# Optimization experiments

Hardware: AMD Instinct MI355X
Metric: run time of the kernel (lower is better)

The kernel has to match this reference:

```python
import jax, jax.numpy as jnp
import numpy as np

B, P, G, E = 2, 16, 128, 96
C110, C011, C001 = 4, 2, 1
N, CO = 128, 2

def _pw(x, W, b):
    """1x1 conv of any spatial rank == pointwise channel mixing."""
    y = jnp.einsum('oc,bc...->bo...', W, x)
    return y + b.reshape((1, -1) + (1,) * (y.ndim - 2))

def _hidden(s110, s011, s001, Ws, bs):
    # s110:[B,C,P,G,1]  s011:[B,C,1,G,E]  s001:[B,C,1,1,E]
    # sub-stream order: [110 full, 110 pool-P, 110 pool-G, 011 full, 011 pool-G, 011 pool-E, 001]
    t110 = s110[..., 0]         # [B,C,P,G]
    t011 = s011[:, :, 0]        # [B,C,G,E]
    t001 = s001[:, :, 0, 0]     # [B,C,E]
    s = (_pw(t110, Ws[0], bs[0])[..., None]
         + _pw(t110.max(axis=2), Ws[1], bs[1])[:, :, None, :, None]
         + _pw(t110.max(axis=3), Ws[2], bs[2])[:, :, :, None, None]
         + _pw(t011, Ws[3], bs[3])[:, :, None, :, :]
         + _pw(t011.max(axis=2), Ws[4], bs[4])[:, :, None, None, :]
         + _pw(t011.max(axis=3), Ws[5], bs[5])[:, :, None, :, None]
         + _pw(t001, Ws[6], bs[6])[:, :, None, None, :])
    s = jax.nn.leaky_relu(s)    # [B,N,P,G,E]
    return (jnp.max(s, axis=4, keepdims=True),
            jnp.max(s, axis=2, keepdims=True),
            jnp.max(s, axis=(2, 3), keepdims=True))

def _forward(x110, x011, x001, W0_110, b0_110, W0_011, b0_011, W0_001, b0_001, W1, b1, Wact, bact, Wcrit, bcrit):
    Ws0 = [W0_110[0], W0_110[1], W0_110[2], W0_011[0], W0_011[1], W0_011[2], W0_001]
    bs0 = [b0_110[0], b0_110[1], b0_110[2], b0_011[0], b0_011[1], b0_011[2], b0_001]
    s110, s011, s001 = _hidden(x110, x011, x001, Ws0, bs0)
    s110, s011, s001 = _hidden(s110, s011, s001, list(W1), list(b1))
    t110 = s110[..., 0]  # [B,N,P,G]
    # actor head: eliminate G,E via mean pooling (dim_elimination_max_pooling=False)
    a110 = _pw(t110.mean(axis=3), Wact[0], bact[0])              # [B,CO,P]
    a011 = _pw(s011.mean(axis=(3, 4)), Wact[1], bact[1])         # [B,CO,1]
    a001 = _pw(s001[:, :, :, 0].mean(axis=3), Wact[2], bact[2])  # [B,CO,1]
    actions = jax.nn.leaky_relu(a110 + a011 + a001)              # [B,CO,P]
    # critic head: eliminate G via mean pooling
    c110 = _pw(t110.mean(axis=3), Wcrit[0], bcrit[0])            # [B,CO,P]
    c011 = _pw(s011[:, :, 0].mean(axis=2), Wcrit[1], bcrit[1])   # [B,CO,E]
    c001 = _pw(s001[:, :, 0, 0], Wcrit[2], bcrit[2])             # [B,CO,E]
    v = jax.nn.leaky_relu(c110[:, :, :, None] + (c011 + c001)[:, :, None, :])  # [B,CO,P,E]
    v110 = v.max(axis=3).sum(axis=2)  # stream (1,1,0): max over E, sum over P
    v011 = v.max(axis=2).sum(axis=2)  # streams (0,1,1) and (0,0,1) coincide numerically
    values = (2.0 + v110 + 2.0 * v011).reshape(-1)  # python sum(l, 2) starts at 2
    return actions, values

def setup_inputs() -> dict:
    key = jax.random.key(0)
    ks = jax.random.split(key, 12)
    f32 = jnp.float32
    def w(k, shape, fan):
        return jax.random.normal(k, shape, f32) / np.float32(np.sqrt(fan))
    return {
        'x110': jax.random.normal(ks[0], (B, C110, P, G, 1), f32),
        'x011': jax.random.normal(ks[1], (B, C011, 1, G, E), f32),
        'x001': jax.random.normal(ks[2], (B, C001, 1, 1, E), f32),
        'W0_110': w(ks[3], (3, N, C110), C110), 'b0_110': jnp.zeros((3, N), f32),
        'W0_011': w(ks[4], (3, N, C011), C011), 'b0_011': jnp.zeros((3, N), f32),
        'W0_001': w(ks[5], (N, C001), C001),    'b0_001': jnp.zeros((N,), f32),
        'W1':     w(ks[6], (7, N, N), N),       'b1':     jnp.zeros((7, N), f32),
        'Wact':   w(ks[7], (3, CO, N), N),      'bact':   jnp.zeros((3, CO), f32),
        'Wcrit':  w(ks[8], (3, CO, N), N),      'bcrit':  jnp.zeros((3, CO), f32),
    }

def reference(x110, x011, x001, W0_110, b0_110, W0_011, b0_011, W0_001, b0_001, W1, b1, Wact, bact, Wcrit, bcrit):
    return _forward(x110, x011, x001, W0_110, b0_110, W0_011, b0_011, W0_001, b0_001, W1, b1, Wact, bact, Wcrit, bcrit)
```

## Files before the change

### kernel.cpp

```cpp
#include <hip/hip_runtime.h>
#include <math.h>

#define DEVI __device__ __forceinline__

constexpr int B = 2, P = 16, G = 128, E = 96, N = 128, CO = 2;

DEVI float lrelu(float x) { return x > 0.f ? x : 0.01f * x; }
DEVI float4 lrelu4(float4 v) {
  return make_float4(lrelu(v.x), lrelu(v.y), lrelu(v.z), lrelu(v.w));
}

constexpr int OFF_U0     = 0;
constexpr int OFF_V0     = OFF_U0 + 524288;
constexpr int OFF_S110   = OFF_V0 + 3145728;
constexpr int OFF_MAXPU0 = OFF_S110 + 524288;
constexpr int OFF_MP110  = OFF_MAXPU0 + 32768;
constexpr int OFF_MG110  = OFF_MP110 + 32768;
constexpr int OFF_S001A  = OFF_MG110 + 4096;
constexpr int OFF_C1P    = OFF_S001A + 24576;
constexpr int OFF_BF1G   = OFF_C1P + 4096;
constexpr int OFF_EG1E   = OFF_BF1G + 32768;
constexpr int OFF_U1     = OFF_EG1E + 24576;
constexpr int OFF_V1     = OFF_U1 + 524288;
constexpr int OFF_M110   = OFF_V1 + 3145728;
constexpr int OFF_M011E  = OFF_M110 + 4096;
constexpr int OFF_S001B  = OFF_M011E + 24576;

__global__ void k_in_reduce(const float* __restrict__ x110,
                            const float* __restrict__ x011,
                            float* __restrict__ rmp110, float* __restrict__ rmg110,
                            float* __restrict__ rme011, float* __restrict__ rmg011) {
  int t = blockIdx.x * 256 + threadIdx.x;
  if (t < 1024) {
    int g = t & 127, c = (t >> 7) & 3, b = t >> 9;
    const float* base = x110 + ((b * 4 + c) * P) * G + g;
    float m = -INFINITY;
    for (int p = 0; p < P; p++) m = fmaxf(m, base[p * G]);
    rmp110[t] = m;
  } else if (t < 1152) {
    int i = t - 1024;
    int p = i & 15, c = (i >> 4) & 3, b = i >> 6;
    const float* base = x110 + ((b * 4 + c) * P + p) * G;
    float m = -INFINITY;
    for (int g = 0; g < G; g++) m = fmaxf(m, base[g]);
    rmg110[i] = m;
  } else if (t < 1664) {
    int i = t - 1152;
    int g = i & 127, c = (i >> 7) & 1, b = i >> 8;
    const float* base = x011 + ((b * 2 + c) * G + g) * E;
    float m = -INFINITY;
    for (int e = 0; e < E; e++) m = fmaxf(m, base[e]);
    rme011[i] = m;
  } else if (t < 2048) {
    int i = t - 1664;
    int e = i % 96; int r = i / 96; int c = r & 1, b = r >> 1;
    const float* base = x011 + ((b * 2 + c) * G) * E + e;
    float m = -INFINITY;
    for (int g = 0; g < G; g++) m = fmaxf(m, base[g * E]);
    rmg011[i] = m;
  }
}

__global__ void k_UV0(const float* __restrict__ x110, const float* __restrict__ x011,
                      const float* __restrict__ x001,
                      const float* __restrict__ W0_110, const float* __restrict__ b0_110,
                      const float* __restrict__ W0_011, const float* __restrict__ b0_011,
                      const float* __restrict__ W0_001, const float* __restrict__ b0_001,
                      const float* __restrict__ rmp110, const float* __restrict__ rmg110,
                      const float* __restrict__ rme011, const float* __restrict__ rmg011,
                      float* __restrict__ U, float* __restrict__ V) {
  int blk = blockIdx.x;
  if (blk < 2048) {
    int t = blk * 256 + threadIdx.x;
    int g = t & 127, p = (t >> 7) & 15, n = (t >> 11) & 127, b = t >> 18;
    float acc = b0_110[n] + b0_110[N + n] + b0_110[2 * N + n] + b0_011[2 * N + n];
#pragma unroll
    for (int c = 0; c < 4; c++) {
      acc += W0_110[n * 4 + c]           * x110[((b * 4 + c) * P + p) * G + g];
      acc += W0_110[(N + n) * 4 + c]     * rmp110[(b * 4 + c) * G + g];
      acc += W0_110[(2 * N + n) * 4 + c] * rmg110[(b * 4 + c) * P + p];
    }
#pragma unroll
    for (int c = 0; c < 2; c++)
      acc += W0_011[(2 * N + n) * 2 + c] * rme011[(b * 2 + c) * G + g];
    U[t] = acc;
  } else {
    int t = (blk - 2048) * 256 + threadIdx.x;
    int e = t % 96; int r = t / 96;
    int g = r & 127, n = (r >> 7) & 127, b = r >> 14;
    float acc = b0_011[n] + b0_011[N + n] + b0_001[n];
#pragma unroll
    for (int c = 0; c < 2; c++) {
      acc += W0_011[n * 2 + c]       * x011[((b * 2 + c) * G + g) * E + e];
      acc += W0_011[(N + n) * 2 + c] * rmg011[(b * 2 + c) * E + e];
    }
    acc += W0_001[n] * x001[b * E + e];
    V[t] = acc;
  }
}

__global__ void __launch_bounds__(256) k_post0(
    const float* __restrict__ U, const float* __restrict__ V,
    float* __restrict__ s110, float* __restrict__ maxpU0,
    float* __restrict__ mp110, float* __restrict__ mg110,
    float* __restrict__ s001a) {
  __shared__ float uU[P * G];
  __shared__ float part[256];
  __shared__ float smaxeV[G], smaxpU[G];
  const int bn = blockIdx.x;
  const int tid = threadIdx.x;
  const float4* usrc = (const float4*)(U + (size_t)bn * P * G);
  float4* udst = (float4*)uU;
  udst[tid] = usrc[tid];
  udst[tid + 256] = usrc[tid + 256];
  {
    int g = tid & 127, h = tid >> 7;
    const float* vrow = V + ((size_t)bn * G + g) * E + h * 48;
    float m = -INFINITY;
#pragma unroll
    for (int j = 0; j < 12; j++) {
      float4 v = *(const float4*)(vrow + j * 4);
      m = fmaxf(m, fmaxf(fmaxf(v.x, v.y), fmaxf(v.z, v.w)));
    }
    part[tid] = m;
  }
  __syncthreads();
  if (tid < G) {
    smaxeV[tid] = fmaxf(part[tid], part[tid + 128]);
    float mp = -INFINITY;
    for (int p = 0; p < P; p++) mp = fmaxf(mp, uU[p * G + tid]);
    smaxpU[tid] = mp;
    maxpU0[bn * G + tid] = mp;
  }
  __syncthreads();
  {
    float4* sdst = (float4*)(s110 + (size_t)bn * P * G);
#pragma unroll
    for (int k = 0; k < 2; k++) {
      int i = tid + k * 256;
      int g4 = i & 31;
      float4 u = ((float4*)uU)[i];
      float4 mv = *(float4*)&smaxeV[g4 * 4];
      sdst[i] = make_float4(lrelu(u.x + mv.x), lrelu(u.y + mv.y),
                            lrelu(u.z + mv.z), lrelu(u.w + mv.w));
    }
  }
  if (tid < G)
    mp110[bn * G + tid] = lrelu(smaxpU[tid] + smaxeV[tid]);
  if (tid < P) {
    float mm = -INFINITY;
    for (int g = 0; g < G; g++) mm = fmaxf(mm, uU[tid * G + g] + smaxeV[g]);
    mg110[bn * P + tid] = lrelu(mm);
  }
  if (tid < E) {
    float mm = -INFINITY;
    const float* vcol = V + (size_t)bn * G * E + tid;
    for (int g = 0; g < G; g++) mm = fmaxf(mm, smaxpU[g] + vcol[g * E]);
    s001a[bn * E + tid] = lrelu(mm);
  }
}

__global__ void k_sg(const float* __restrict__ W1, const float* __restrict__ mp110,
                     const float* __restrict__ mg110, const float* __restrict__ s001a,
                     float* __restrict__ C1p, float* __restrict__ BF1g,
                     float* __restrict__ EG1e) {
  int t = blockIdx.x * 256 + threadIdx.x;
  if (t < 4096) {
    int p = t & 15, n = (t >> 4) & 127, b = t >> 11;
    float acc = 0.f;
    for (int c = 0; c < N; c++)
      acc += W1[(2 * N + n) * N + c] * mg110[(b * N + c) * P + p];
    C1p[t] = acc;
  } else if (t < 36864) {
    int i = t - 4096;
    int g = i & 127, n = (i >> 7) & 127, b = i >> 14;
    float acc = 0.f;
    for (int c = 0; c < N; c++)
      acc += (W1[(1 * N + n) * N + c] + W1[(5 * N + n) * N + c])
             * mp110[(b * N + c) * G + g];
    BF1g[i] = acc;
  } else {
    int i = t - 36864;
    int e = i % 96; int r = i / 96; int n = r & 127, b = r >> 7;
    float acc = 0.f;
    for (int c = 0; c < N; c++)
      acc += (W1[(4 * N + n) * N + c] + W1[(6 * N + n) * N + c])
             * s001a[(b * N + c) * E + e];
    EG1e[i] = acc;
  }
}

__global__ void __launch_bounds__(256) k_V1U1(
    const float* __restrict__ V0, const float* __restrict__ maxpU0,
    const float* __restrict__ s110, const float* __restrict__ W1,
    const float* __restrict__ b1, const float* __restrict__ C1p,
    const float* __restrict__ BF1g, const float* __restrict__ EG1e,
    float* __restrict__ U1, float* __restrict__ V1) {
  __shared__ float sS[N * E];
  const int blk = blockIdx.x;
  const int tid = threadIdx.x;
  if (blk < 256) {
    const int g = blk & 127, b = blk >> 7;
    for (int i4 = tid; i4 < N * E / 4; i4 += 256) {
      int c = i4 / 24, e4 = i4 - c * 24;
      float4 v = *(const float4*)(V0 + ((size_t)(b * N + c) * G + g) * E + e4 * 4);
      float mp = maxpU0[(b * N + c) * G + g];
      *(float4*)&sS[c * E + e4 * 4] =
          make_float4(lrelu(v.x + mp), lrelu(v.y + mp),
                      lrelu(v.z + mp), lrelu(v.w + mp));
    }
    __syncthreads();
    const int e12 = tid & 7, n4 = tid >> 3;
    const int n0 = n4 * 4, e0 = e12 * 12;
    float4 acc[4][3];
#pragma unroll
    for (int ni = 0; ni < 4; ni++) {
      int n = n0 + ni;
      float bb = b1[3 * N + n] + b1[4 * N + n] + b1[6 * N + n];
      const float* eg = EG1e + (b * N + n) * E + e0;
#pragma unroll
      for (int k = 0; k < 3; k++)
        acc[ni][k] = make_float4(bb + eg[k * 4], bb + eg[k * 4 + 1],
                                 bb + eg[k * 4 + 2], bb + eg[k * 4 + 3]);
    }
    for (int c = 0; c < N; c += 4) {
      float4 wv[4];
#pragma unroll
      for (int ni = 0; ni < 4; ni++)
        wv[ni] = *(const float4*)&W1[(size_t)(3 * N + n0 + ni) * N + c];
#pragma unroll
      for (int cc = 0; cc < 4; cc++) {
        float4 s0 = *(float4*)&sS[(c + cc) * E + e0];
        float4 s1 = *(float4*)&sS[(c + cc) * E + e0 + 4];
        float4 s2 = *(float4*)&sS[(c + cc) * E + e0 + 8];
#pragma unroll
        for (int ni = 0; ni < 4; ni++) {
          float wc = cc == 0 ? wv[ni].x : cc == 1 ? wv[ni].y : cc == 2 ? wv[ni].z : wv[ni].w;
          acc[ni][0].x += wc * s0.x; acc[ni][0].y += wc * s0.y;
          acc[ni][0].z += wc * s0.z; acc[ni][0].w += wc * s0.w;
          acc[ni][1].x += wc * s1.x; acc[ni][1].y += wc * s1.y;
          acc[ni][1].z += wc * s1.z; acc[ni][1].w += wc * s1.w;
          acc[ni][2].x += wc * s2.x; acc[ni][2].y += wc * s2.y;
          acc[ni][2].z += wc * s2.z; acc[ni][2].w += wc * s2.w;
        }
      }
    }
#pragma unroll
    for (int ni = 0; ni < 4; ni++) {
      float* dst = V1 + ((size_t)(b * N + n0 + ni) * G + g) * E + e0;
#pragma unroll
      for (int k = 0; k < 3; k++) *(float4*)(dst + k * 4) = acc[ni][k];
    }
  } else {
    int t = (blk - 256) * 256 + tid;
    int g4 = t & 31, p = (t >> 5) & 15, n4 = (t >> 9) & 31, b = t >> 14;
    int n0 = n4 * 4;
    float4 a[4];
#pragma unroll
    for (int ni = 0; ni < 4; ni++) {
      int n = n0 + ni;
      float bb = b1[n] + b1[N + n] + b1[2 * N + n] + b1[5 * N + n]
               + C1p[(b * N + n) * P + p];
      float4 bf = *(const float4*)&BF1g[(b * N + n) * G + g4 * 4];
      a[ni] = make_float4(bb + bf.x, bb + bf.y, bb + bf.z, bb + bf.w);
    }
#pragma unroll 4
    for (int c = 0; c < N; c++) {
      float4 v = *(const float4*)&s110[((size_t)(b * N + c) * P + p) * G + g4 * 4];
#pragma unroll
      for (int ni = 0; ni < 4; ni++) {
        float wc = W1[(size_t)(n0 + ni) * N + c];
        a[ni].x += wc * v.x; a[ni].y += wc * v.y;
        a[ni].z += wc * v.z; a[ni].w += wc * v.w;
      }
    }
#pragma unroll
    for (int ni = 0; ni < 4; ni++)
      *(float4*)&U1[((size_t)(b * N + n0 + ni) * P + p) * G + g4 * 4] = a[ni];
  }
}

__global__ void __launch_bounds__(256) k_post1(
    const float* __restrict__ U1, const float* __restrict__ V1,
    float* __restrict__ m110, float* __restrict__ m011e,
    float* __restrict__ s001b) {
  __shared__ float uU[P * G];
  __shared__ float part[256];
  __shared__ float smaxeV[G], smaxpU[G];
  const int bn = blockIdx.x;
  const int tid = threadIdx.x;
  const float4* usrc = (const float4*)(U1 + (size_t)bn * P * G);
  float4* udst = (float4*)uU;
  udst[tid] = usrc[tid];
  udst[tid + 256] = usrc[tid + 256];
  {
    int g = tid & 127, h = tid >> 7;
    const float* vrow = V1 + ((size_t)bn * G + g) * E + h * 48;
    float m = -INFINITY;
#pragma unroll
    for (int j = 0; j < 12; j++) {
      float4 v = *(const float4*)(vrow + j * 4);
      m = fmaxf(m, fmaxf(fmaxf(v.x, v.y), fmaxf(v.z, v.w)));
    }
    part[tid] = m;
  }
  __syncthreads();
  if (tid < G) {
    smaxeV[tid] = fmaxf(part[tid], part[tid + 128]);
    float mp = -INFINITY;
    for (int p = 0; p < P; p++) mp = fmaxf(mp, uU[p * G + tid]);
    smaxpU[tid] = mp;
  }
  __syncthreads();
  if (tid < P) {
    float s = 0.f;
    for (int g = 0; g < G; g++) s += lrelu(uU[tid * G + g] + smaxeV[g]);
    m110[bn * P + tid] = s * (1.f / G);
  }
  if (tid < E) {
    float s = 0.f, mm = -INFINITY;
    const float* vcol = V1 + (size_t)bn * G * E + tid;
    for (int g = 0; g < G; g++) {
      float pre = smaxpU[g] + vcol[g * E];
      s += lrelu(pre);
      mm = fmaxf(mm, pre);
    }
    m011e[bn * E + tid] = s * (1.f / G);
    s001b[bn * E + tid] = lrelu(mm);
  }
}

__global__ void __launch_bounds__(128) k_final(const float* __restrict__ m110,
                                               const float* __restrict__ m011e,
                                               const float* __restrict__ s001,
                                               const float* __restrict__ Wact,
                                               const float* __restrict__ bact,
                                               const float* __restrict__ Wcrit,
                                               const float* __restrict__ bcrit,
                                               float* __restrict__ out) {
  __shared__ float sm011[N], sm001[N], scp[P], sce[E], srow[P], scol[E];
  const int bo = blockIdx.x;
  const int o = bo & 1, b = bo >> 1;
  const int t = threadIdx.x;
  {
    float s1 = 0.f, s2 = 0.f;
    const float* p1 = m011e + (b * N + t) * E;
    const float* p2 = s001 + (b * N + t) * E;
    for (int e = 0; e < E; e++) { s1 += p1[e]; s2 += p2[e]; }
    sm011[t] = s1 * (1.f / E);
    sm001[t] = s2 * (1.f / E);
  }
  __syncthreads();
  if (t < P) {
    const float* wa0 = Wact + o * N;
    const float* wa1 = Wact + (1 * CO + o) * N;
    const float* wa2 = Wact + (2 * CO + o) * N;
    const float* wc0 = Wcrit + o * N;
    float a = 0.f, c = 0.f, aa = 0.f;
    for (int n = 0; n < N; n++) {
      float m = m110[(b * N + n) * P + t];
      a += wa0[n] * m;
      c += wc0[n] * m;
      aa += wa1[n] * sm011[n] + wa2[n] * sm001[n];
    }
    float act = a + aa + bact[o] + bact[CO + o] + bact[2 * CO + o];
    out[(b * CO + o) * P + t] = lrelu(act);
    scp[t] = c + bcrit[o];
  } else if (t < P + E) {
    int e = t - P;
    const float* wc1 = Wcrit + (1 * CO + o) * N;
    const float* wc2 = Wcrit + (2 * CO + o) * N;
    float c = 0.f;
    for (int n = 0; n < N; n++)
      c += wc1[n] * m011e[(b * N + n) * E + e] + wc2[n] * s001[(b * N + n) * E + e];
    sce[e] = c + bcrit[CO + o] + bcrit[2 * CO + o];
  }
  __syncthreads();
  if (t < P) {
    float m = -INFINITY;
    for (int e = 0; e < E; e++) m = fmaxf(m, lrelu(scp[t] + sce[e]));
    srow[t] = m;
  } else if (t < P + E) {
    int e = t - P;
    float m = -INFINITY;
    for (int p = 0; p < P; p++) m = fmaxf(m, lrelu(scp[p] + sce[e]));
    scol[e] = m;
  }
  __syncthreads();
  if (t == 0) {
    float v110 = 0.f, v011 = 0.f;
    for (int p = 0; p < P; p++) v110 += srow[p];
    for (int e = 0; e < E; e++) v011 += scol[e];
    out[B * CO * P + b * CO + o] = 2.f + v110 + 2.f * v011;
  }
}

extern "C" void kernel_launch(void* const* d_in, const int* in_sizes, int n_in,
                              void* d_out, int out_size, void* d_ws, size_t ws_size,
                              hipStream_t stream) {
  const float* x110   = (const float*)d_in[0];
  const float* x011   = (const float*)d_in[1];
  const float* x001   = (const float*)d_in[2];
  const float* W0_110 = (const float*)d_in[3];
  const float* b0_110 = (const float*)d_in[4];
  const float* W0_011 = (const float*)d_in[5];
  const float* b0_011 = (const float*)d_in[6];
  const float* W0_001 = (const float*)d_in[7];
  const float* b0_001 = (const float*)d_in[8];
  const float* W1     = (const float*)d_in[9];
  const float* b1     = (const float*)d_in[10];
  const float* Wact   = (const float*)d_in[11];
  const float* bact   = (const float*)d_in[12];
  const float* Wcrit  = (const float*)d_in[13];
  const float* bcrit  = (const float*)d_in[14];
  float* out = (float*)d_out;
  float* w = (float*)d_ws;

  float* U0     = w + OFF_U0;
  float* V0     = w + OFF_V0;
  float* s110   = w + OFF_S110;
  float* maxpU0 = w + OFF_MAXPU0;
  float* mp110  = w + OFF_MP110;
  float* mg110  = w + OFF_MG110;
  float* s001a  = w + OFF_S001A;
  float* C1p    = w + OFF_C1P;
  float* BF1g   = w + OFF_BF1G;
  float* EG1e   = w + OFF_EG1E;
  float* U1     = w + OFF_U1;
  float* V1     = w + OFF_V1;
  float* m110   = w + OFF_M110;
  float* m011e  = w + OFF_M011E;
  float* s001b  = w + OFF_S001B;

  float* rmp110 = w + OFF_S001B + 24576;
  float* rmg110 = rmp110 + 1024;
  float* rme011 = rmg110 + 128;
  float* rmg011 = rme011 + 512;

  k_in_reduce<<<8, 256, 0, stream>>>(x110, x011, rmp110, rmg110, rme011, rmg011);
  k_UV0<<<14336, 256, 0, stream>>>(x110, x011, x001, W0_110, b0_110, W0_011,
                                   b0_011, W0_001, b0_001,
                                   rmp110, rmg110, rme011, rmg011, U0, V0);
  k_post0<<<256, 256, 0, stream>>>(U0, V0, s110, maxpU0, mp110, mg110, s001a);
  k_sg<<<240, 256, 0, stream>>>(W1, mp110, mg110, s001a, C1p, BF1g, EG1e);
  k_V1U1<<<384, 256, 0, stream>>>(V0, maxpU0, s110, W1, b1, C1p, BF1g, EG1e,
                                  U1, V1);
  k_post1<<<256, 256, 0, stream>>>(U1, V1, m110, m011e, s001b);
  k_final<<<4, 128, 0, stream>>>(m110, m011e, s001b, Wact, bact, Wcrit, bcrit, out);
}
```

Before: 125.7 us.

## Fuse layer-0 into per-(b,n) blocks and recompute layer-0 activations in layer-1

Merges the input reductions, the layer-0 pointwise U0/V0 computation and its post-processing into one kernel, so each (b,n) block builds U0/V0 in shared memory instead of writing them to global memory. The layer-1 kernel now regenerates the needed s110 and s011 slices per (b,g) from the raw inputs and the stored max vectors rather than reading the large V0 and s110 buffers. This removes roughly 15 MB of global writes and reads and two launches. In exchange the layer-0 arithmetic is recomputed, and the shared-memory footprint grows, which may limit occupancy. The U1 store is also changed to a strided scalar pattern.

Result: faster. 104.7 us (-16.7%).

```diff
diff --git a/kernel.cpp b/kernel.cpp
--- a/kernel.cpp
+++ b/kernel.cpp
@@ -6,157 +6,162 @@
 constexpr int B = 2, P = 16, G = 128, E = 96, N = 128, CO = 2;
 
 DEVI float lrelu(float x) { return x > 0.f ? x : 0.01f * x; }
-DEVI float4 lrelu4(float4 v) {
-  return make_float4(lrelu(v.x), lrelu(v.y), lrelu(v.z), lrelu(v.w));
-}
-
-constexpr int OFF_U0     = 0;
-constexpr int OFF_V0     = OFF_U0 + 524288;
-constexpr int OFF_S110   = OFF_V0 + 3145728;
-constexpr int OFF_MAXPU0 = OFF_S110 + 524288;
-constexpr int OFF_MP110  = OFF_MAXPU0 + 32768;
+
+constexpr int OFF_U1     = 0;
+constexpr int OFF_V1     = OFF_U1 + 524288;
+constexpr int OFF_MAXPU0 = OFF_V1 + 3145728;
+constexpr int OFF_MAXEV0 = OFF_MAXPU0 + 32768;
+constexpr int OFF_MP110  = OFF_MAXEV0 + 32768;
 constexpr int OFF_MG110  = OFF_MP110 + 32768;
 constexpr int OFF_S001A  = OFF_MG110 + 4096;
-constexpr int OFF_C1P    = OFF_S001A + 24576;
+constexpr int OFF_RMP    = OFF_S001A + 24576;
+constexpr int OFF_RMG    = OFF_RMP + 1024;
+constexpr int OFF_RME    = OFF_RMG + 128;
+constexpr int OFF_RMG011 = OFF_RME + 512;
+constexpr int OFF_C1P    = OFF_RMG011 + 384;
 constexpr int OFF_BF1G   = OFF_C1P + 4096;
 constexpr int OFF_EG1E   = OFF_BF1G + 32768;
-constexpr int OFF_U1     = OFF_EG1E + 24576;
-constexpr int OFF_V1     = OFF_U1 + 524288;
-constexpr int OFF_M110   = OFF_V1 + 3145728;
+constexpr int OFF_M110   = OFF_EG1E + 24576;
 constexpr int OFF_M011E  = OFF_M110 + 4096;
 constexpr int OFF_S001B  = OFF_M011E + 24576;
 
-__global__ void k_in_reduce(const float* __restrict__ x110,
-                            const float* __restrict__ x011,
-                            float* __restrict__ rmp110, float* __restrict__ rmg110,
-                            float* __restrict__ rme011, float* __restrict__ rmg011) {
-  int t = blockIdx.x * 256 + threadIdx.x;
-  if (t < 1024) {
-    int g = t & 127, c = (t >> 7) & 3, b = t >> 9;
-    const float* base = x110 + ((b * 4 + c) * P) * G + g;
-    float m = -INFINITY;
-    for (int p = 0; p < P; p++) m = fmaxf(m, base[p * G]);
-    rmp110[t] = m;
-  } else if (t < 1152) {
-    int i = t - 1024;
-    int p = i & 15, c = (i >> 4) & 3, b = i >> 6;
-    const float* base = x110 + ((b * 4 + c) * P + p) * G;
-    float m = -INFINITY;
-    for (int g = 0; g < G; g++) m = fmaxf(m, base[g]);
-    rmg110[i] = m;
-  } else if (t < 1664) {
-    int i = t - 1152;
-    int g = i & 127, c = (i >> 7) & 1, b = i >> 8;
-    const float* base = x011 + ((b * 2 + c) * G + g) * E;
-    float m = -INFINITY;
-    for (int e = 0; e < E; e++) m = fmaxf(m, base[e]);
-    rme011[i] = m;
-  } else if (t < 2048) {
-    int i = t - 1664;
-    int e = i % 96; int r = i / 96; int c = r & 1, b = r >> 1;
-    const float* base = x011 + ((b * 2 + c) * G) * E + e;
-    float m = -INFINITY;
-    for (int g = 0; g < G; g++) m = fmaxf(m, base[g * E]);
-    rmg011[i] = m;
-  }
-}
-
-__global__ void k_UV0(const float* __restrict__ x110, const float* __restrict__ x011,
-                      const float* __restrict__ x001,
-                      const float* __restrict__ W0_110, const float* __restrict__ b0_110,
-                      const float* __restrict__ W0_011, const float* __restrict__ b0_011,
-                      const float* __restrict__ W0_001, const float* __restrict__ b0_001,
-                      const float* __restrict__ rmp110, const float* __restrict__ rmg110,
-                      const float* __restrict__ rme011, const float* __restrict__ rmg011,
-                      float* __restrict__ U, float* __restrict__ V) {
-  int blk = blockIdx.x;
-  if (blk < 2048) {
-    int t = blk * 256 + threadIdx.x;
-    int g = t & 127, p = (t >> 7) & 15, n = (t >> 11) & 127, b = t >> 18;
-    float acc = b0_110[n] + b0_110[N + n] + b0_110[2 * N + n] + b0_011[2 * N + n];
-#pragma unroll
-    for (int c = 0; c < 4; c++) {
-      acc += W0_110[n * 4 + c]           * x110[((b * 4 + c) * P + p) * G + g];
-      acc += W0_110[(N + n) * 4 + c]     * rmp110[(b * 4 + c) * G + g];
-      acc += W0_110[(2 * N + n) * 4 + c] * rmg110[(b * 4 + c) * P + p];
-    }
-#pragma unroll
-    for (int c = 0; c < 2; c++)
-      acc += W0_011[(2 * N + n) * 2 + c] * rme011[(b * 2 + c) * G + g];
-    U[t] = acc;
-  } else {
-    int t = (blk - 2048) * 256 + threadIdx.x;
-    int e = t % 96; int r = t / 96;
-    int g = r & 127, n = (r >> 7) & 127, b = r >> 14;
-    float acc = b0_011[n] + b0_011[N + n] + b0_001[n];
-#pragma unroll
-    for (int c = 0; c < 2; c++) {
-      acc += W0_011[n * 2 + c]       * x011[((b * 2 + c) * G + g) * E + e];
-      acc += W0_011[(N + n) * 2 + c] * rmg011[(b * 2 + c) * E + e];
-    }
-    acc += W0_001[n] * x001[b * E + e];
-    V[t] = acc;
-  }
-}
-
-__global__ void __launch_bounds__(256) k_post0(
-    const float* __restrict__ U, const float* __restrict__ V,
-    float* __restrict__ s110, float* __restrict__ maxpU0,
+__global__ void __launch_bounds__(256) k_layer0(
+    const float* __restrict__ x110, const float* __restrict__ x011,
+    const float* __restrict__ x001,
+    const float* __restrict__ W0_110, const float* __restrict__ b0_110,
+    const float* __restrict__ W0_011, const float* __restrict__ b0_011,
+    const float* __restrict__ W0_001, const float* __restrict__ b0_001,
+    float* __restrict__ maxpU0g, float* __restrict__ maxeV0g,
     float* __restrict__ mp110, float* __restrict__ mg110,
-    float* __restrict__ s001a) {
-  __shared__ float uU[P * G];
-  __shared__ float part[256];
-  __shared__ float smaxeV[G], smaxpU[G];
-  const int bn = blockIdx.x;
-  const int tid = threadIdx.x;
-  const float4* usrc = (const float4*)(U + (size_t)bn * P * G);
-  float4* udst = (float4*)uU;
-  udst[tid] = usrc[tid];
-  udst[tid + 256] = usrc[tid + 256];
+    float* __restrict__ s001a,
+    float* __restrict__ rmpG, float* __restrict__ rmgG,
+    float* __restrict__ rmeG, float* __restrict__ rmg011G) {
+  __shared__ float xs[4 * 16 * 128];
+  __shared__ float v0[128 * 97];
+  __shared__ float u0[16 * 128];
+  __shared__ float rmp[4 * 128], rmgS[4 * 16], rme[2 * 128], rmg011L[2 * 96];
+  __shared__ float mpu[128], mev[128], part[256];
+  const int bn = blockIdx.x, b = bn >> 7, n = bn & 127, tid = threadIdx.x;
+
+  {
+    const float4* xsrc = (const float4*)(x110 + (size_t)b * 8192);
+    float4* xdst = (float4*)xs;
+#pragma unroll
+    for (int k = 0; k < 8; k++) xdst[tid + k * 256] = xsrc[tid + k * 256];
+  }
+  __syncthreads();
+  for (int i = tid; i < 512; i += 256) {
+    int c = i >> 7, g = i & 127;
+    float m = -INFINITY;
+    for (int p = 0; p < P; p++) m = fmaxf(m, xs[(c * 16 + p) * 128 + g]);
+    rmp[i] = m;
+  }
+  if (tid < 64) {
+    int c = tid >> 4, p = tid & 15;
+    float m = -INFINITY;
+    for (int g = 0; g < G; g++) m = fmaxf(m, xs[(c * 16 + p) * 128 + g]);
+    rmgS[tid] = m;
+  }
+  {
+    int c = tid >> 7, g = tid & 127;
+    const float4* r = (const float4*)(x011 + ((size_t)(b * 2 + c) * 128 + g) * 96);
+    float m = -INFINITY;
+#pragma unroll
+    for (int j = 0; j < 24; j++) {
+      float4 v = r[j];
+      m = fmaxf(m, fmaxf(fmaxf(v.x, v.y), fmaxf(v.z, v.w)));
+    }
+    rme[tid] = m;
+  }
+  if (tid < 192) {
+    int c = tid / 96, e = tid % 96;
+    const float* pp = x011 + ((size_t)(b * 2 + c) * 128) * 96 + e;
+    float m = -INFINITY;
+    for (int g = 0; g < G; g++) m = fmaxf(m, pp[g * 96]);
+    rmg011L[tid] = m;
+  }
+  __syncthreads();
+  float w0[4], w1[4], w2[4];
+#pragma unroll
+  for (int cc = 0; cc < 4; cc++) {
+    w0[cc] = W0_110[n * 4 + cc];
+    w1[cc] = W0_110[512 + n * 4 + cc];
+    w2[cc] = W0_110[1024 + n * 4 + cc];
+  }
+  float we0 = W0_011[512 + n * 2], we1 = W0_011[512 + n * 2 + 1];
+  float bu = b0_110[n] + b0_110[128 + n] + b0_110[256 + n] + b0_011[256 + n];
+  float vw00 = W0_011[n * 2], vw01 = W0_011[n * 2 + 1];
+  float vw10 = W0_011[256 + n * 2], vw11 = W0_011[256 + n * 2 + 1];
+  float w001 = W0_001[n];
+  float bv = b0_011[n] + b0_011[128 + n] + b0_001[n];
+
+#pragma unroll
+  for (int k = 0; k < 8; k++) {
+    int i = tid + k * 256, p = i >> 7, g = i & 127;
+    float acc = bu + we0 * rme[g] + we1 * rme[128 + g];
+#pragma unroll
+    for (int cc = 0; cc < 4; cc++)
+      acc += w0[cc] * xs[(cc * 16 + p) * 128 + g] + w1[cc] * rmp[cc * 128 + g]
+           + w2[cc] * rmgS[cc * 16 + p];
+    u0[i] = acc;
+  }
+  {
+    const float* xa = x011 + (size_t)(b * 2) * 12288;
+    const float* xb = xa + 12288;
+    const float* xc = x001 + b * 96;
+    for (int k = 0; k < 48; k++) {
+      int i = tid + k * 256;
+      int g = i / 96, e = i - g * 96;
+      float val = bv + vw00 * xa[i] + vw01 * xb[i]
+                + vw10 * rmg011L[e] + vw11 * rmg011L[96 + e] + w001 * xc[e];
+      v0[g * 97 + e] = val;
+    }
+  }
+  __syncthreads();
+  if (tid < 128) {
+    float m = -INFINITY;
+    for (int p = 0; p < P; p++) m = fmaxf(m, u0[p * 128 + tid]);
+    mpu[tid] = m;
+    maxpU0g[bn * 128 + tid] = m;
+  }
   {
     int g = tid & 127, h = tid >> 7;
-    const float* vrow = V + ((size_t)bn * G + g) * E + h * 48;
-    float m = -INFINITY;
-#pragma unroll
-    for (int j = 0; j < 12; j++) {
-      float4 v = *(const float4*)(vrow + j * 4);
-      m = fmaxf(m, fmaxf(fmaxf(v.x, v.y), fmaxf(v.z, v.w)));
-    }
+    const float* r = &v0[g * 97 + h * 48];
+    float m = -INFINITY;
+    for (int j = 0; j < 48; j++) m = fmaxf(m, r[j]);
     part[tid] = m;
   }
   __syncthreads();
-  if (tid < G) {
-    smaxeV[tid] = fmaxf(part[tid], part[tid + 128]);
-    float mp = -INFINITY;
-    for (int p = 0; p < P; p++) mp = fmaxf(mp, uU[p * G + tid]);
-    smaxpU[tid] = mp;
-    maxpU0[bn * G + tid] = mp;
-  }
-  __syncthreads();
-  {
-    float4* sdst = (float4*)(s110 + (size_t)bn * P * G);
-#pragma unroll
-    for (int k = 0; k < 2; k++) {
-      int i = tid + k * 256;
-      int g4 = i & 31;
-      float4 u = ((float4*)uU)[i];
-      float4 mv = *(float4*)&smaxeV[g4 * 4];
-      sdst[i] = make_float4(lrelu(u.x + mv.x), lrelu(u.y + mv.y),
-                            lrelu(u.z + mv.z), lrelu(u.w + mv.w));
-    }
-  }
-  if (tid < G)
-    mp110[bn * G + tid] = lrelu(smaxpU[tid] + smaxeV[tid]);
-  if (tid < P) {
-    float mm = -INFINITY;
-    for (int g = 0; g < G; g++) mm = fmaxf(mm, uU[tid * G + g] + smaxeV[g]);
-    mg110[bn * P + tid] = lrelu(mm);
-  }
-  if (tid < E) {
-    float mm = -INFINITY;
-    const float* vcol = V + (size_t)bn * G * E + tid;
-    for (int g = 0; g < G; g++) mm = fmaxf(mm, smaxpU[g] + vcol[g * E]);
-    s001a[bn * E + tid] = lrelu(mm);
+  if (tid < 128) {
+    float m = fmaxf(part[tid], part[128 + tid]);
+    mev[tid] = m;
+    maxeV0g[bn * 128 + tid] = m;
+    mp110[bn * 128 + tid] = lrelu(mpu[tid] + m);
+  }
+  __syncthreads();
+  {
+    int p = tid >> 4, ch = tid & 15;
+    float m = -INFINITY;
+    for (int g = ch * 8; g < ch * 8 + 8; g++)
+      m = fmaxf(m, u0[p * 128 + g] + mev[g]);
+    part[tid] = m;
+  }
+  if (tid < 96) {
+    float m = -INFINITY;
+    for (int g = 0; g < G; g++) m = fmaxf(m, mpu[g] + v0[g * 97 + tid]);
+    s001a[bn * 96 + tid] = lrelu(m);
+  }
+  __syncthreads();
+  if (tid < 16) {
+    float m = -INFINITY;
+    for (int ch = 0; ch < 16; ch++) m = fmaxf(m, part[tid * 16 + ch]);
+    mg110[bn * 16 + tid] = lrelu(m);
+  }
+  if (n == 0) {
+    for (int i = tid; i < 512; i += 256) rmpG[b * 512 + i] = rmp[i];
+    if (tid < 64) rmgG[b * 64 + tid] = rmgS[tid];
+    rmeG[b * 256 + tid] = rme[tid];
+    if (tid < 192) rmg011G[b * 192 + tid] = rmg011L[tid];
   }
 }
 
@@ -190,93 +195,131 @@
   }
 }
 
-__global__ void __launch_bounds__(256) k_V1U1(
-    const float* __restrict__ V0, const float* __restrict__ maxpU0,
-    const float* __restrict__ s110, const float* __restrict__ W1,
-    const float* __restrict__ b1, const float* __restrict__ C1p,
-    const float* __restrict__ BF1g, const float* __restrict__ EG1e,
+__global__ void __launch_bounds__(256) k_layer1(
+    const float* __restrict__ x110, const float* __restrict__ x011,
+    const float* __restrict__ x001,
+    const float* __restrict__ W0_110, const float* __restrict__ b0_110,
+    const float* __restrict__ W0_011, const float* __restrict__ b0_011,
+    const float* __restrict__ W0_001, const float* __restrict__ b0_001,
+    const float* __restrict__ maxpU0g, const float* __restrict__ maxeV0g,
+    const float* __restrict__ rmpG, const float* __restrict__ rmgG,
+    const float* __restrict__ rmeG, const float* __restrict__ rmg011G,
+    const float* __restrict__ W1, const float* __restrict__ b1,
+    const float* __restrict__ C1p, const float* __restrict__ BF1g,
+    const float* __restrict__ EG1e,
     float* __restrict__ U1, float* __restrict__ V1) {
-  __shared__ float sS[N * E];
+  __shared__ float s110c[128 * 16];
+  __shared__ float s011c[128 * 96];
+  __shared__ float W0L110[1536], W0L011[768], W0L001[128];
+  __shared__ float busum[128], bvsum[128], mpu[128], mev[128];
+  __shared__ float x011row[192], rmg011s[192], x001s[96];
+  __shared__ float x110col[64], rmg110p[64], rmp4[4], rme2[2];
   const int blk = blockIdx.x;
+  const int b = blk >> 8, g = (blk >> 1) & 127, nh = blk & 1;
+  const int n0 = nh * 64;
   const int tid = threadIdx.x;
-  if (blk < 256) {
-    const int g = blk & 127, b = blk >> 7;
-    for (int i4 = tid; i4 < N * E / 4; i4 += 256) {
-      int c = i4 / 24, e4 = i4 - c * 24;
-      float4 v = *(const float4*)(V0 + ((size_t)(b * N + c) * G + g) * E + e4 * 4);
-      float mp = maxpU0[(b * N + c) * G + g];
-      *(float4*)&sS[c * E + e4 * 4] =
-          make_float4(lrelu(v.x + mp), lrelu(v.y + mp),
-                      lrelu(v.z + mp), lrelu(v.w + mp));
-    }
-    __syncthreads();
-    const int e12 = tid & 7, n4 = tid >> 3;
-    const int n0 = n4 * 4, e0 = e12 * 12;
-    float4 acc[4][3];
-#pragma unroll
-    for (int ni = 0; ni < 4; ni++) {
-      int n = n0 + ni;
-      float bb = b1[3 * N + n] + b1[4 * N + n] + b1[6 * N + n];
-      const float* eg = EG1e + (b * N + n) * E + e0;
-#pragma unroll
-      for (int k = 0; k < 3; k++)
-        acc[ni][k] = make_float4(bb + eg[k * 4], bb + eg[k * 4 + 1],
-                                 bb + eg[k * 4 + 2], bb + eg[k * 4 + 3]);
-    }
-    for (int c = 0; c < N; c += 4) {
-      float4 wv[4];
-#pragma unroll
-      for (int ni = 0; ni < 4; ni++)
-        wv[ni] = *(const float4*)&W1[(size_t)(3 * N + n0 + ni) * N + c];
-#pragma unroll
-      for (int cc = 0; cc < 4; cc++) {
-        float4 s0 = *(float4*)&sS[(c + cc) * E + e0];
-        float4 s1 = *(float4*)&sS[(c + cc) * E + e0 + 4];
-        float4 s2 = *(float4*)&sS[(c + cc) * E + e0 + 8];
-#pragma unroll
-        for (int ni = 0; ni < 4; ni++) {
-          float wc = cc == 0 ? wv[ni].x : cc == 1 ? wv[ni].y : cc == 2 ? wv[ni].z : wv[ni].w;
-          acc[ni][0].x += wc * s0.x; acc[ni][0].y += wc * s0.y;
-          acc[ni][0].z += wc * s0.z; acc[ni][0].w += wc * s0.w;
-          acc[ni][1].x += wc * s1.x; acc[ni][1].y += wc * s1.y;
-          acc[ni][1].z += wc * s1.z; acc[ni][1].w += wc * s1.w;
-          acc[ni][2].x += wc * s2.x; acc[ni][2].y += wc * s2.y;
-          acc[ni][2].z += wc * s2.z; acc[ni][2].w += wc * s2.w;
-        }
+
+  for (int i = tid; i < 1536; i += 256) W0L110[i] = W0_110[i];
+  for (int i = tid; i < 768; i += 256) W0L011[i] = W0_011[i];
+  if (tid < 128) {
+    W0L001[tid] = W0_001[tid];
+    busum[tid] = b0_110[tid] + b0_110[128 + tid] + b0_110[256 + tid] + b0_011[256 + tid];
+    bvsum[tid] = b0_011[tid] + b0_011[128 + tid] + b0_001[tid];
+    mpu[tid] = maxpU0g[(b * 128 + tid) * 128 + g];
+    mev[tid] = maxeV0g[(b * 128 + tid) * 128 + g];
+  }
+  if (tid < 192) {
+    int c = tid / 96, e = tid % 96;
+    x011row[tid] = x011[((size_t)(b * 2 + c) * 128 + g) * 96 + e];
+    rmg011s[tid] = rmg011G[b * 192 + tid];
+  }
+  if (tid < 96) x001s[tid] = x001[b * 96 + tid];
+  if (tid < 64) {
+    int c = tid >> 4, p = tid & 15;
+    x110col[tid] = x110[((size_t)(b * 4 + c) * 16 + p) * 128 + g];
+    rmg110p[tid] = rmgG[b * 64 + tid];
+  }
+  if (tid < 4) rmp4[tid] = rmpG[(b * 4 + tid) * 128 + g];
+  if (tid < 2) rme2[tid] = rmeG[(b * 2 + tid) * 128 + g];
+  __syncthreads();
+
+#pragma unroll
+  for (int k = 0; k < 8; k++) {
+    int i = tid + k * 256, c = i >> 4, p = i & 15;
+    float acc = busum[c] + W0L011[512 + c * 2] * rme2[0]
+              + W0L011[512 + c * 2 + 1] * rme2[1];
+#pragma unroll
+    for (int cc = 0; cc < 4; cc++)
+      acc += W0L110[c * 4 + cc] * x110col[cc * 16 + p]
+           + W0L110[512 + c * 4 + cc] * rmp4[cc]
+           + W0L110[1024 + c * 4 + cc] * rmg110p[cc * 16 + p];
+    s110c[i] = lrelu(acc + mev[c]);
+  }
+  for (int k = 0; k < 48; k++) {
+    int i = tid + k * 256;
+    int c = i / 96, e = i - c * 96;
+    float v = bvsum[c] + W0L011[c * 2] * x011row[e] + W0L011[c * 2 + 1] * x011row[96 + e]
+            + W0L011[256 + c * 2] * rmg011s[e] + W0L011[256 + c * 2 + 1] * rmg011s[96 + e]
+            + W0L001[c] * x001s[e];
+    s011c[i] = lrelu(v + mpu[c]);
+  }
+  __syncthreads();
+
+  {
+    int nn = tid >> 2, pq = tid & 3;
+    int n = n0 + nn;
+    float bb = b1[n] + b1[128 + n] + b1[256 + n] + b1[640 + n]
+             + BF1g[(b * 128 + n) * 128 + g];
+    float4 cp = *(const float4*)&C1p[(b * 128 + n) * 16 + pq * 4];
+    float4 a = make_float4(bb + cp.x, bb + cp.y, bb + cp.z, bb + cp.w);
+    const float* wr = W1 + (size_t)n * 128;
+    for (int c = 0; c < 128; c++) {
+      float wv = wr[c];
+      float4 s = *(const float4*)&s110c[c * 16 + pq * 4];
+      a.x += wv * s.x; a.y += wv * s.y; a.z += wv * s.z; a.w += wv * s.w;
+    }
+    float* dst = U1 + ((size_t)(b * 128 + n) * 16 + pq * 4) * 128 + g;
+    dst[0] = a.x; dst[128] = a.y; dst[256] = a.z; dst[384] = a.w;
+  }
+  {
+    int n2 = tid >> 3, e0 = (tid & 7) * 12;
+    int na = n0 + n2 * 2, nb = na + 1;
+    float4 aA[3], aB[3];
+    {
+      float bbA = b1[384 + na] + b1[512 + na] + b1[768 + na];
+      float bbB = b1[384 + nb] + b1[512 + nb] + b1[768 + nb];
+      const float* egA = EG1e + (b * 128 + na) * 96 + e0;
+      const float* egB = EG1e + (b * 128 + nb) * 96 + e0;
+#pragma unroll
+      for (int k = 0; k < 3; k++) {
+        aA[k] = make_float4(bbA + egA[k * 4], bbA + egA[k * 4 + 1],
+                            bbA + egA[k * 4 + 2], bbA + egA[k * 4 + 3]);
+        aB[k] = make_float4(bbB + egB[k * 4], bbB + egB[k * 4 + 1],
+                            bbB + egB[k * 4 + 2], bbB + egB[k * 4 + 3]);
       }
     }
-#pragma unroll
-    for (int ni = 0; ni < 4; ni++) {
-      float* dst = V1 + ((size_t)(b * N + n0 + ni) * G + g) * E + e0;
-#pragma unroll
-      for (int k = 0; k < 3; k++) *(float4*)(dst + k * 4) = acc[ni][k];
-    }
-  } else {
-    int t = (blk - 256) * 256 + tid;
-    int g4 = t & 31, p = (t >> 5) & 15, n4 = (t >> 9) & 31, b = t >> 14;
-    int n0 = n4 * 4;
-    float4 a[4];
-#pragma unroll
-    for (int ni = 0; ni < 4; ni++) {
-      int n = n0 + ni;
-      float bb = b1[n] + b1[N + n] + b1[2 * N + n] + b1[5 * N + n]
-               + C1p[(b * N + n) * P + p];
-      float4 bf = *(const float4*)&BF1g[(b * N + n) * G + g4 * 4];
-      a[ni] = make_float4(bb + bf.x, bb + bf.y, bb + bf.z, bb + bf.w);
-    }
+    const float* wA = W1 + (size_t)(384 + na) * 128;
+    const float* wB = W1 + (size_t)(384 + nb) * 128;
 #pragma unroll 4
-    for (int c = 0; c < N; c++) {
-      float4 v = *(const float4*)&s110[((size_t)(b * N + c) * P + p) * G + g4 * 4];
-#pragma unroll
-      for (int ni = 0; ni < 4; ni++) {
-        float wc = W1[(size_t)(n0 + ni) * N + c];
-        a[ni].x += wc * v.x; a[ni].y += wc * v.y;
-        a[ni].z += wc * v.z; a[ni].w += wc * v.w;
-      }
-    }
-#pragma unroll
-    for (int ni = 0; ni < 4; ni++)
-      *(float4*)&U1[((size_t)(b * N + n0 + ni) * P + p) * G + g4 * 4] = a[ni];
+    for (int c = 0; c < 128; c++) {
+      float4 s0 = *(const float4*)&s011c[c * 96 + e0];
+      float4 s1 = *(const float4*)&s011c[c * 96 + e0 + 4];
+      float4 s2 = *(const float4*)&s011c[c * 96 + e0 + 8];
+      float wa = wA[c], wb = wB[c];
+      aA[0].x += wa * s0.x; aA[0].y += wa * s0.y; aA[0].z += wa * s0.z; aA[0].w += wa * s0.w;
+      aA[1].x += wa * s1.x; aA[1].y += wa * s1.y; aA[1].z += wa * s1.z; aA[1].w += wa * s1.w;
+      aA[2].x += wa * s2.x; aA[2].y += wa * s2.y; aA[2].z += wa * s2.z; aA[2].w += wa * s2.w;
+      aB[0].x += wb * s0.x; aB[0].y += wb * s0.y; aB[0].z += wb * s0.z; aB[0].w += wb * s0.w;
+      aB[1].x += wb * s1.x; aB[1].y += wb * s1.y; aB[1].z += wb * s1.z; aB[1].w += wb * s1.w;
+      aB[2].x += wb * s2.x; aB[2].y += wb * s2.y; aB[2].z += wb * s2.z; aB[2].w += wb * s2.w;
+    }
+    float* dA = V1 + ((size_t)(b * 128 + na) * 128 + g) * 96 + e0;
+    float* dB = V1 + ((size_t)(b * 128 + nb) * 128 + g) * 96 + e0;
+#pragma unroll
+    for (int k = 0; k < 3; k++) {
+      *(float4*)(dA + k * 4) = aA[k];
+      *(float4*)(dB + k * 4) = aB[k];
+    }
   }
 }
 
@@ -416,35 +459,33 @@
   float* out = (float*)d_out;
   float* w = (float*)d_ws;
 
-  float* U0     = w + OFF_U0;
-  float* V0     = w + OFF_V0;
-  float* s110   = w + OFF_S110;
+  float* U1     = w + OFF_U1;
+  float* V1     = w + OFF_V1;
   float* maxpU0 = w + OFF_MAXPU0;
+  float* maxeV0 = w + OFF_MAXEV0;
   float* mp110  = w + OFF_MP110;
   float* mg110  = w + OFF_MG110;
   float* s001a  = w + OFF_S001A;
+  float* rmpG   = w + OFF_RMP;
+  float* rmgG   = w + OFF_RMG;
+  float* rmeG   = w + OFF_RME;
+  float* rmg011 = w + OFF_RMG011;
   float* C1p    = w + OFF_C1P;
   float* BF1g   = w + OFF_BF1G;
   float* EG1e   = w + OFF_EG1E;
-  float* U1     = w + OFF_U1;
-  float* V1     = w + OFF_V1;
   float* m110   = w + OFF_M110;
   float* m011e  = w + OFF_M011E;
   float* s001b  = w + OFF_S001B;
 
-  float* rmp110 = w + OFF_S001B + 24576;
-  float* rmg110 = rmp110 + 1024;
-  float* rme011 = rmg110 + 128;
-  float* rmg011 = rme011 + 512;
-
-  k_in_reduce<<<8, 256, 0, stream>>>(x110, x011, rmp110, rmg110, rme011, rmg011);
-  k_UV0<<<14336, 256, 0, stream>>>(x110, x011, x001, W0_110, b0_110, W0_011,
-                                   b0_011, W0_001, b0_001,
-                                   rmp110, rmg110, rme011, rmg011, U0, V0);
-  k_post0<<<256, 256, 0, stream>>>(U0, V0, s110, maxpU0, mp110, mg110, s001a);
+  k_layer0<<<256, 256, 0, stream>>>(x110, x011, x001, W0_110, b0_110, W0_011,
+                                    b0_011, W0_001, b0_001,
+                                    maxpU0, maxeV0, mp110, mg110, s001a,
+                                    rmpG, rmgG, rmeG, rmg011);
   k_sg<<<240, 256, 0, stream>>>(W1, mp110, mg110, s001a, C1p, BF1g, EG1e);
-  k_V1U1<<<384, 256, 0, stream>>>(V0, maxpU0, s110, W1, b1, C1p, BF1g, EG1e,
-                                  U1, V1);
+  k_layer1<<<512, 256, 0, stream>>>(x110, x011, x001, W0_110, b0_110, W0_011,
+                                    b0_011, W0_001, b0_001,
+                                    maxpU0, maxeV0, rmpG, rmgG, rmeG, rmg011,
+                                    W1, b1, C1p, BF1g, EG1e, U1, V1);
   k_post1<<<256, 256, 0, stream>>>(U1, V1, m110, m011e, s001b);
   k_final<<<4, 128, 0, stream>>>(m110, m011e, s001b, Wact, bact, Wcrit, bcrit, out);
 }
```
